# Performance work log

Measured on AMD Instinct MI355X. Metric: run time of the kernel, lower is better.

## Reference

```python
import jax, jax.numpy as jnp
import numpy as np

N_ATOMS = 50000
N_EDGES = 640000
D = 128
N_RBF = 20
N_INTER = 3

act = jax.nn.softplus


def setup_inputs() -> dict:
    key = jax.random.key(0)
    ks = jax.random.split(key, 16)
    s = 1.0 / np.sqrt(D)
    inp = {
        "x": jax.random.normal(ks[0], (N_ATOMS, D), jnp.float32),
        "g_ij": jax.random.uniform(ks[1], (N_EDGES, N_RBF), jnp.float32),
        "idx_i": jax.random.randint(ks[2], (N_EDGES,), 0, N_ATOMS),
        "idx_j": jax.random.randint(ks[3], (N_EDGES,), 0, N_ATOMS),
        "n_atoms": N_ATOMS,
        "u": jnp.ones((D,), jnp.float32),
        "Wf": jax.random.normal(ks[4], (D, D), jnp.float32) * s,
        "bf": jnp.zeros((D,), jnp.float32),
        # linear_g weight init to zero in original; use small random so grads flow
        "Wg": jax.random.normal(ks[5], (D, N_RBF), jnp.float32) * 0.01,
        "bg": jnp.zeros((D,), jnp.float32),
        "Wj": jax.random.normal(ks[6], (D, D), jnp.float32) * s,
        "bj": jnp.zeros((D,), jnp.float32),
        "Wi": jax.random.normal(ks[7], (D, D), jnp.float32) * s,
        "bi": jnp.zeros((D,), jnp.float32),
        "res_w1": jax.random.normal(ks[8], (N_INTER, D, D), jnp.float32) * s,
        "res_b1": jnp.zeros((N_INTER, D), jnp.float32),
        "res_w2": jax.random.normal(ks[9], (N_INTER, D, D), jnp.float32) * s,
        "res_b2": jnp.zeros((N_INTER, D), jnp.float32),
    }
    return inp


def reference(x, g_ij, idx_i, idx_j, n_atoms, u, Wf, bf, Wg, bg, Wj, bj, Wi, bi,
              res_w1, res_b1, res_w2, res_b2):
    x_j = x[idx_j]                                    # [E, D] gather
    xp = u * x                                        # [N, D]
    # sequential_j: act -> linear_j -> act, gated by linear_g(g_ij)
    vp = act(act(x_j) @ Wj.T + bj) * (g_ij @ Wg.T + bg)   # [E, D]
    vm = act(act(x) @ Wi.T + bi)                      # [N, D]
    v = jax.ops.segment_sum(vp, idx_i, num_segments=n_atoms) + vm
    for l in range(res_w1.shape[0]):
        h = act(v) @ res_w1[l].T + res_b1[l]
        h = act(h) @ res_w2[l].T + res_b2[l]
        v = h + v
    v = act(v)
    return xp + v @ Wf.T + bf
```

## Files before the change

### kernel.cpp

```cpp
#include <hip/hip_runtime.h>

#define DD 128

typedef __attribute__((ext_vector_type(8))) short short8;
typedef __attribute__((ext_vector_type(8))) unsigned short ushort8;
typedef __attribute__((ext_vector_type(4))) float floatx4;
typedef unsigned int uint32;

__device__ __forceinline__ float sp(float x) {
    return fmaxf(x, 0.0f) + __logf(1.0f + __expf(-fabsf(x)));
}

__device__ __forceinline__ unsigned short f2bf(float f) {
    union { float f; uint32 u; } c; c.f = f;
    const uint32 u = c.u;
    return (unsigned short)((u + 0x7fffu + ((u >> 16) & 1u)) >> 16);
}

__global__ __launch_bounds__(256)
void convert_w(const float* __restrict__ Wj, const float* __restrict__ Wi,
               const float* __restrict__ rw1, const float* __restrict__ rw2,
               const float* __restrict__ Wf, unsigned short* __restrict__ out)
{
    const int gid = blockIdx.x * 256 + threadIdx.x;
    if (gid >= 9 * 2048) return;
    const int mat = gid >> 11;
    const int f8  = gid & 2047;
    const float* src;
    if      (mat == 0) src = Wj;
    else if (mat == 1) src = Wi;
    else if (mat <= 4) src = rw1 + (size_t)(mat - 2) * 16384;
    else if (mat <= 7) src = rw2 + (size_t)(mat - 5) * 16384;
    else               src = Wf;
    const int row = f8 >> 4;
    const int ch  = f8 & 15;
    const float4 a = reinterpret_cast<const float4*>(src)[2 * f8];
    const float4 b = reinterpret_cast<const float4*>(src)[2 * f8 + 1];
    ushort8 u8;
    u8[0] = f2bf(a.x); u8[1] = f2bf(a.y); u8[2] = f2bf(a.z); u8[3] = f2bf(a.w);
    u8[4] = f2bf(b.x); u8[5] = f2bf(b.y); u8[6] = f2bf(b.z); u8[7] = f2bf(b.w);
    *reinterpret_cast<ushort8*>(out + (size_t)mat * 16384 + row * 128 +
                                ((ch ^ (row & 15)) << 3)) = u8;
}

__device__ __forceinline__ void stage_wb(const unsigned short* __restrict__ Wb,
                                         unsigned short* wl, int t)
{
    #pragma unroll
    for (int i = 0; i < 8; ++i) {
        const int c = t + i * 256;
        *reinterpret_cast<ushort8*>(wl + c * 8) =
            *reinterpret_cast<const ushort8*>(Wb + c * 8);
    }
}

__device__ __forceinline__ void load_afrag_act(const float* __restrict__ X,
                                               int m, int q, int n, short8 af[4])
{
    const int mm = m < n ? m : n - 1;
    const float* row = X + (size_t)mm * DD + q * 8;
    #pragma unroll
    for (int kk = 0; kk < 4; ++kk) {
        const float4 a = *reinterpret_cast<const float4*>(row + kk * 32);
        const float4 b = *reinterpret_cast<const float4*>(row + kk * 32 + 4);
        ushort8 u;
        u[0] = f2bf(sp(a.x)); u[1] = f2bf(sp(a.y)); u[2] = f2bf(sp(a.z)); u[3] = f2bf(sp(a.w));
        u[4] = f2bf(sp(b.x)); u[5] = f2bf(sp(b.y)); u[6] = f2bf(sp(b.z)); u[7] = f2bf(sp(b.w));
        af[kk] = __builtin_bit_cast(short8, u);
    }
}

__device__ __forceinline__ void mfma_gemm(const unsigned short* wl,
                                          const short8 af[4],
                                          int cl, int q, floatx4 acc[8])
{
    #pragma unroll
    for (int nt = 0; nt < 8; ++nt) {
        const int nrow = nt * 16 + cl;
        #pragma unroll
        for (int kk = 0; kk < 4; ++kk) {
            const int chs = (kk * 4 + q) ^ cl;
            const short8 bfr = *reinterpret_cast<const short8*>(wl + nrow * 128 + (chs << 3));
            acc[nt] = __builtin_amdgcn_mfma_f32_16x16x32_bf16(af[kk], bfr, acc[nt], 0, 0, 0);
        }
    }
}

__global__ __launch_bounds__(256, 4)
void dual_gemm(const float* __restrict__ x,
               const unsigned short* __restrict__ Wb,
               const float* __restrict__ bj, const float* __restrict__ bi,
               unsigned short* __restrict__ Aout, float* __restrict__ vout, int n)
{
    __shared__ __align__(16) unsigned short wl[128 * 128];
    const int t = threadIdx.x;
    const int lane = t & 63, wv = t >> 6;
    const int cl = lane & 15, q = lane >> 4;
    const int m0 = blockIdx.x * 64 + wv * 16;

    short8 af[4];
    load_afrag_act(x, m0 + cl, q, n, af);

    stage_wb(Wb, wl, t);
    __syncthreads();

    floatx4 acc[8];
    #pragma unroll
    for (int nt = 0; nt < 8; ++nt) acc[nt] = (floatx4){0.f, 0.f, 0.f, 0.f};
    mfma_gemm(wl, af, cl, q, acc);

    #pragma unroll
    for (int nt = 0; nt < 8; ++nt) {
        const int col = nt * 16 + cl;
        const float bb = bj[col];
        #pragma unroll
        for (int r = 0; r < 4; ++r) {
            const int row = m0 + q * 4 + r;
            if (row < n) Aout[(size_t)row * DD + col] = f2bf(sp(acc[nt][r] + bb));
        }
    }

    __syncthreads();
    stage_wb(Wb + 16384, wl, t);
    __syncthreads();

    #pragma unroll
    for (int nt = 0; nt < 8; ++nt) acc[nt] = (floatx4){0.f, 0.f, 0.f, 0.f};
    mfma_gemm(wl, af, cl, q, acc);

    #pragma unroll
    for (int nt = 0; nt < 8; ++nt) {
        const int col = nt * 16 + cl;
        const float bb = bi[col];
        #pragma unroll
        for (int r = 0; r < 4; ++r) {
            const int row = m0 + q * 4 + r;
            if (row < n) vout[(size_t)row * DD + col] = sp(acc[nt][r] + bb);
        }
    }
}

__global__ __launch_bounds__(256, 2)
void tail_kernel(const float* __restrict__ vin, const float* __restrict__ x,
                 const unsigned short* __restrict__ Wb,
                 const float* __restrict__ rb1, const float* __restrict__ rb2,
                 const float* __restrict__ bf, const float* __restrict__ u,
                 float* __restrict__ out, int n)
{
    __shared__ __align__(16) unsigned short wl[128 * 128];
    __shared__ __align__(16) unsigned short hl[64 * 128];
    __shared__ __align__(16) float vt[64 * 128];
    const int t = threadIdx.x;
    const int lane = t & 63, wv = t >> 6;
    const int cl = lane & 15, q = lane >> 4;
    const int mb = blockIdx.x * 64;

    #pragma unroll
    for (int i = 0; i < 8; ++i) {
        const int c = t + i * 256;
        const int row = c >> 5;
        const int chv = c & 31;
        float4 val = make_float4(0.f, 0.f, 0.f, 0.f);
        if (mb + row < n) val = reinterpret_cast<const float4*>(vin)[(size_t)mb * 32 + c];
        *reinterpret_cast<float4*>(vt + row * 128 + ((chv ^ (row & 15)) << 2)) = val;
    }
    stage_wb(Wb + 2 * 16384, wl, t);
    __syncthreads();

    floatx4 vac[8];
    #pragma unroll
    for (int nt = 0; nt < 8; ++nt) {
        #pragma unroll
        for (int r = 0; r < 4; ++r) {
            const int rl = wv * 16 + q * 4 + r;
            const int col = nt * 16 + cl;
            const int chv = col >> 2;
            vac[nt][r] = vt[rl * 128 + ((chv ^ (rl & 15)) << 2) + (col & 3)];
        }
    }

    short8 af[4];
    {
        const int rl = wv * 16 + cl;
        #pragma unroll
        for (int kk = 0; kk < 4; ++kk) {
            const int c0 = q * 2 + kk * 8;
            const floatx4 A0 = *reinterpret_cast<const floatx4*>(vt + rl * 128 + (((c0    ) ^ cl) << 2));
            const floatx4 A1 = *reinterpret_cast<const floatx4*>(vt + rl * 128 + (((c0 + 1) ^ cl) << 2));
            ushort8 u8;
            u8[0] = f2bf(sp(A0[0])); u8[1] = f2bf(sp(A0[1])); u8[2] = f2bf(sp(A0[2])); u8[3] = f2bf(sp(A0[3]));
            u8[4] = f2bf(sp(A1[0])); u8[5] = f2bf(sp(A1[1])); u8[6] = f2bf(sp(A1[2])); u8[7] = f2bf(sp(A1[3]));
            af[kk] = __builtin_bit_cast(short8, u8);
        }
    }

    const int ml2 = wv * 16 + cl;

    for (int l = 0; l < 3; ++l) {
        if (l > 0) {
            #pragma unroll
            for (int nt = 0; nt < 8; ++nt) {
                const int col = nt * 16 + cl;
                const int ch = col >> 3;
                #pragma unroll
                for (int r = 0; r < 4; ++r) {
                    const int ml = wv * 16 + q * 4 + r;
                    hl[ml * 128 + ((ch ^ (ml & 15)) << 3) + (col & 7)] = f2bf(sp(vac[nt][r]));
                }
            }
            #pragma unroll
            for (int kk = 0; kk < 4; ++kk)
                af[kk] = *reinterpret_cast<const short8*>(hl + ml2 * 128 + (((kk * 4 + q) ^ cl) << 3));
            __syncthreads();
            stage_wb(Wb + (size_t)(2 + l) * 16384, wl, t);
            __syncthreads();
        }

        floatx4 acc[8];
        #pragma unroll
        for (int nt = 0; nt < 8; ++nt) acc[nt] = (floatx4){0.f, 0.f, 0.f, 0.f};
        mfma_gemm(wl, af, cl, q, acc);

        const float* b1 = rb1 + (size_t)l * DD;
        #pragma unroll
        for (int nt = 0; nt < 8; ++nt) {
            const int col = nt * 16 + cl;
            const int ch = col >> 3;
            const float bb = b1[col];
            #pragma unroll
            for (int r = 0; r < 4; ++r) {
                const int ml = wv * 16 + q * 4 + r;
                hl[ml * 128 + ((ch ^ (ml & 15)) << 3) + (col & 7)] = f2bf(sp(acc[nt][r] + bb));
            }
        }
        short8 af2[4];
        #pragma unroll
        for (int kk = 0; kk < 4; ++kk)
            af2[kk] = *reinterpret_cast<const short8*>(hl + ml2 * 128 + (((kk * 4 + q) ^ cl) << 3));

        __syncthreads();
        stage_wb(Wb + (size_t)(5 + l) * 16384, wl, t);
        __syncthreads();

        #pragma unroll
        for (int nt = 0; nt < 8; ++nt) acc[nt] = (floatx4){0.f, 0.f, 0.f, 0.f};
        mfma_gemm(wl, af2, cl, q, acc);

        const float* b2 = rb2 + (size_t)l * DD;
        #pragma unroll
        for (int nt = 0; nt < 8; ++nt) {
            const float bb = b2[nt * 16 + cl];
            #pragma unroll
            for (int r = 0; r < 4; ++r) vac[nt][r] += acc[nt][r] + bb;
        }
    }

    __syncthreads();
    stage_wb(Wb + (size_t)8 * 16384, wl, t);
    #pragma unroll
    for (int i = 0; i < 8; ++i) {
        const int c = t + i * 256;
        const int row = c >> 5;
        const int chv = c & 31;
        float4 val = make_float4(0.f, 0.f, 0.f, 0.f);
        if (mb + row < n) val = reinterpret_cast<const float4*>(x)[(size_t)mb * 32 + c];
        *reinterpret_cast<float4*>(vt + row * 128 + ((chv ^ (row & 15)) << 2)) = val;
    }
    __syncthreads();

    #pragma unroll
    for (int nt = 0; nt < 8; ++nt) {
        const int col = nt * 16 + cl;
        const int ch = col >> 3;
        #pragma unroll
        for (int r = 0; r < 4; ++r) {
            const int ml = wv * 16 + q * 4 + r;
            hl[ml * 128 + ((ch ^ (ml & 15)) << 3) + (col & 7)] = f2bf(sp(vac[nt][r]));
        }
    }
    short8 aff[4];
    #pragma unroll
    for (int kk = 0; kk < 4; ++kk)
        aff[kk] = *reinterpret_cast<const short8*>(hl + ml2 * 128 + (((kk * 4 + q) ^ cl) << 3));

    floatx4 acc[8];
    #pragma unroll
    for (int nt = 0; nt < 8; ++nt) acc[nt] = (floatx4){0.f, 0.f, 0.f, 0.f};
    mfma_gemm(wl, aff, cl, q, acc);

    #pragma unroll
    for (int nt = 0; nt < 8; ++nt) {
        const int col = nt * 16 + cl;
        const float bb = bf[col];
        const float uu = u[col];
        const int chv = col >> 2;
        #pragma unroll
        for (int r = 0; r < 4; ++r) {
            const int rl = wv * 16 + q * 4 + r;
            const int row = mb + rl;
            if (row < n) {
                const float xv = vt[rl * 128 + ((chv ^ (rl & 15)) << 2) + (col & 3)];
                out[(size_t)row * DD + col] = acc[nt][r] + bb + uu * xv;
            }
        }
    }
}


__global__ __launch_bounds__(256)
void hist_kernel(const int* __restrict__ idx_i, int* __restrict__ cnt, int E)
{
    const int e = blockIdx.x * 256 + threadIdx.x;
    if (e < E) atomicAdd(&cnt[idx_i[e]], 1);
}

__global__ __launch_bounds__(256)
void scan_reduce(const int* __restrict__ cnt, int* __restrict__ bsum, int n)
{
    __shared__ int wsum[4];
    const int t = threadIdx.x;
    const int lane = t & 63, wv = t >> 6;
    const int i0 = blockIdx.x * 1024 + t * 4;
    int s = 0;
    #pragma unroll
    for (int k = 0; k < 4; ++k) if (i0 + k < n) s += cnt[i0 + k];
    #pragma unroll
    for (int d = 1; d < 64; d <<= 1) s += __shfl_down(s, d, 64);
    if (lane == 0) wsum[wv] = s;
    __syncthreads();
    if (t == 0) bsum[blockIdx.x] = wsum[0] + wsum[1] + wsum[2] + wsum[3];
}

__global__ __launch_bounds__(64)
void scan_partials(int* __restrict__ bsum, int nb)
{
    const int t = threadIdx.x;
    int v = (t < nb) ? bsum[t] : 0;
    int incl = v;
    #pragma unroll
    for (int d = 1; d < 64; d <<= 1) {
        const int y = __shfl_up(incl, d, 64);
        if (t >= d) incl += y;
    }
    if (t < nb) bsum[t] = incl - v;
}

__global__ __launch_bounds__(256)
void scan_apply(const int* __restrict__ cnt, const int* __restrict__ bsum,
                int* __restrict__ off, int* __restrict__ cnt2, int n)
{
    __shared__ int wsum[4];
    const int t = threadIdx.x;
    const int lane = t & 63, wv = t >> 6;
    const int i0 = blockIdx.x * 1024 + t * 4;
    const int v0 = (i0 + 0 < n) ? cnt[i0 + 0] : 0;
    const int v1 = (i0 + 1 < n) ? cnt[i0 + 1] : 0;
    const int v2 = (i0 + 2 < n) ? cnt[i0 + 2] : 0;
    const int v3 = (i0 + 3 < n) ? cnt[i0 + 3] : 0;
    const int s = v0 + v1 + v2 + v3;
    int incl = s;
    #pragma unroll
    for (int d = 1; d < 64; d <<= 1) {
        const int y = __shfl_up(incl, d, 64);
        if (lane >= d) incl += y;
    }
    if (lane == 63) wsum[wv] = incl;
    __syncthreads();
    int woff = bsum[blockIdx.x];
    #pragma unroll
    for (int w = 0; w < 4; ++w) if (w < wv) woff += wsum[w];
    const int excl = woff + incl - s;
    if (i0 + 0 < n) { off[i0 + 0] = excl;                cnt2[i0 + 0] = 0; }
    if (i0 + 1 < n) { off[i0 + 1] = excl + v0;           cnt2[i0 + 1] = 0; }
    if (i0 + 2 < n) { off[i0 + 2] = excl + v0 + v1;      cnt2[i0 + 2] = 0; }
    if (i0 + 3 < n) { off[i0 + 3] = excl + v0 + v1 + v2; cnt2[i0 + 3] = 0; }
}

__global__ __launch_bounds__(256)
void scatter_kernel(const int* __restrict__ idx_i, const int* __restrict__ idx_j,
                    const int* __restrict__ off, int* __restrict__ cnt2,
                    int2* __restrict__ spair, int E)
{
    const int e = blockIdx.x * 256 + threadIdx.x;
    if (e < E) {
        const int i = idx_i[e];
        const int p = off[i] + atomicAdd(&cnt2[i], 1);
        spair[p] = make_int2(e, idx_j[e]);
    }
}

__global__ __launch_bounds__(256, 4)
void agg_kernel(const int* __restrict__ off, const int* __restrict__ cnt,
                const int2* __restrict__ spair,
                const float* __restrict__ g,
                const float* __restrict__ Wg, const float* __restrict__ bg,
                const unsigned short* __restrict__ A, float* __restrict__ v, int N)
{
    const int t = threadIdx.x;
    const int lane = t & 63;
    const int wid0 = blockIdx.x * 4 + (t >> 6);
    const int nw   = gridDim.x * 4;
    const int d0 = lane << 1;

    float2 wg01[20];
    #pragma unroll
    for (int k = 0; k < 20; ++k) {
        wg01[k].x = Wg[d0 * 20 + k];
        wg01[k].y = Wg[(d0 + 1) * 20 + k];
    }
    const float bg0 = bg[d0], bg1 = bg[d0 + 1];

    for (int i = wid0; i < N; i += nw) {
        const int beg = off[i], num = cnt[i], end = beg + num;

        float2 acc = *reinterpret_cast<const float2*>(v + (size_t)i * DD + d0);

        int p = beg;
        for (; p + 2 <= end; p += 2) {
            const int2 pr0 = spair[p];
            const int2 pr1 = spair[p + 1];
            const int e0 = __builtin_amdgcn_readfirstlane(pr0.x);
            const int j0 = __builtin_amdgcn_readfirstlane(pr0.y);
            const int e1 = __builtin_amdgcn_readfirstlane(pr1.x);
            const int j1 = __builtin_amdgcn_readfirstlane(pr1.y);
            const uint32 a0 = *reinterpret_cast<const uint32*>(A + (size_t)j0 * DD + d0);
            const uint32 a1 = *reinterpret_cast<const uint32*>(A + (size_t)j1 * DD + d0);
            const float4* g0p = reinterpret_cast<const float4*>(g + (size_t)e0 * 20);
            const float4* g1p = reinterpret_cast<const float4*>(g + (size_t)e1 * 20);
            float2 t0 = make_float2(bg0, bg1), t1 = make_float2(bg0, bg1);
            #pragma unroll
            for (int qq = 0; qq < 5; ++qq) {
                const float4 p0 = g0p[qq];
                const float4 p1 = g1p[qq];
                t0.x = fmaf(p0.x, wg01[qq*4+0].x, t0.x); t0.y = fmaf(p0.x, wg01[qq*4+0].y, t0.y);
                t0.x = fmaf(p0.y, wg01[qq*4+1].x, t0.x); t0.y = fmaf(p0.y, wg01[qq*4+1].y, t0.y);
                t0.x = fmaf(p0.z, wg01[qq*4+2].x, t0.x); t0.y = fmaf(p0.z, wg01[qq*4+2].y, t0.y);
                t0.x = fmaf(p0.w, wg01[qq*4+3].x, t0.x); t0.y = fmaf(p0.w, wg01[qq*4+3].y, t0.y);
                t1.x = fmaf(p1.x, wg01[qq*4+0].x, t1.x); t1.y = fmaf(p1.x, wg01[qq*4+0].y, t1.y);
                t1.x = fmaf(p1.y, wg01[qq*4+1].x, t1.x); t1.y = fmaf(p1.y, wg01[qq*4+1].y, t1.y);
                t1.x = fmaf(p1.z, wg01[qq*4+2].x, t1.x); t1.y = fmaf(p1.z, wg01[qq*4+2].y, t1.y);
                t1.x = fmaf(p1.w, wg01[qq*4+3].x, t1.x); t1.y = fmaf(p1.w, wg01[qq*4+3].y, t1.y);
            }
            union { uint32 u; float f; } c0x, c0y, c1x, c1y;
            c0x.u = a0 << 16; c0y.u = a0 & 0xffff0000u;
            c1x.u = a1 << 16; c1y.u = a1 & 0xffff0000u;
            acc.x = fmaf(c0x.f, t0.x, acc.x); acc.y = fmaf(c0y.f, t0.y, acc.y);
            acc.x = fmaf(c1x.f, t1.x, acc.x); acc.y = fmaf(c1y.f, t1.y, acc.y);
        }
        if (p < end) {
            const int2 pr0 = spair[p];
            const int e0 = __builtin_amdgcn_readfirstlane(pr0.x);
            const int j0 = __builtin_amdgcn_readfirstlane(pr0.y);
            const uint32 a0 = *reinterpret_cast<const uint32*>(A + (size_t)j0 * DD + d0);
            const float4* g0p = reinterpret_cast<const float4*>(g + (size_t)e0 * 20);
            float2 t0 = make_float2(bg0, bg1);
            #pragma unroll
            for (int qq = 0; qq < 5; ++qq) {
                const float4 p0 = g0p[qq];
                t0.x = fmaf(p0.x, wg01[qq*4+0].x, t0.x); t0.y = fmaf(p0.x, wg01[qq*4+0].y, t0.y);
                t0.x = fmaf(p0.y, wg01[qq*4+1].x, t0.x); t0.y = fmaf(p0.y, wg01[qq*4+1].y, t0.y);
                t0.x = fmaf(p0.z, wg01[qq*4+2].x, t0.x); t0.y = fmaf(p0.z, wg01[qq*4+2].y, t0.y);
                t0.x = fmaf(p0.w, wg01[qq*4+3].x, t0.x); t0.y = fmaf(p0.w, wg01[qq*4+3].y, t0.y);
            }
            union { uint32 u; float f; } c0x, c0y;
            c0x.u = a0 << 16; c0y.u = a0 & 0xffff0000u;
            acc.x = fmaf(c0x.f, t0.x, acc.x); acc.y = fmaf(c0y.f, t0.y, acc.y);
        }
        *reinterpret_cast<float2*>(v + (size_t)i * DD + d0) = acc;
    }
}

extern "C" void kernel_launch(void* const* d_in, const int* in_sizes, int n_in,
                              void* d_out, int out_size, void* d_ws, size_t ws_size,
                              hipStream_t stream)
{
    const float* x     = (const float*)d_in[0];
    const float* g     = (const float*)d_in[1];
    const int*   idx_i = (const int*)d_in[2];
    const int*   idx_j = (const int*)d_in[3];
    const float* u     = (const float*)d_in[5];
    const float* Wf    = (const float*)d_in[6];
    const float* bf    = (const float*)d_in[7];
    const float* Wg    = (const float*)d_in[8];
    const float* bg    = (const float*)d_in[9];
    const float* Wj    = (const float*)d_in[10];
    const float* bj    = (const float*)d_in[11];
    const float* Wi    = (const float*)d_in[12];
    const float* bi    = (const float*)d_in[13];
    const float* rw1   = (const float*)d_in[14];
    const float* rb1   = (const float*)d_in[15];
    const float* rw2   = (const float*)d_in[16];
    const float* rb2   = (const float*)d_in[17];

    const int N = in_sizes[0] / DD;
    const int E = in_sizes[2];
    float* out = (float*)d_out;

    float*          v     = (float*)d_ws;
    unsigned short* A     = (unsigned short*)(v + (size_t)N * DD);
    int*            cnt   = (int*)(A + (size_t)N * DD);
    int*            off   = cnt + N;
    int*            cnt2  = off + N;
    int*            bsum  = cnt2 + N;
    int2*           spair = (int2*)(bsum + 64);
    unsigned short* Wb    = (unsigned short*)(spair + E);

    dim3 blk(256);
    const int tiles    = (N + 63) / 64;
    const int eblocks  = (E + 255) / 256;
    const int sblocks  = (N + 1023) / 1024;

    convert_w<<<72, blk, 0, stream>>>(Wj, Wi, rw1, rw2, Wf, Wb);

    hipMemsetAsync(cnt, 0, (size_t)N * sizeof(int), stream);
    hist_kernel<<<eblocks, blk, 0, stream>>>(idx_i, cnt, E);
    scan_reduce<<<sblocks, blk, 0, stream>>>(cnt, bsum, N);
    scan_partials<<<1, 64, 0, stream>>>(bsum, sblocks);
    scan_apply<<<sblocks, blk, 0, stream>>>(cnt, bsum, off, cnt2, N);
    scatter_kernel<<<eblocks, blk, 0, stream>>>(idx_i, idx_j, off, cnt2, spair, E);

    dual_gemm<<<tiles, blk, 0, stream>>>(x, Wb, bj, bi, A, v, N);

    agg_kernel<<<2048, blk, 0, stream>>>(off, cnt, spair, g, Wg, bg, A, v, N);

    tail_kernel<<<tiles, blk, 0, stream>>>(v, x, Wb, rb1, rb2, bf, u, out, N);
}
```

Measured before the change: 255.5 us.

## Store g_ij as fp16 and compute the edge gate with packed half FMAs

New measurement: 242.7 us. 1.05x faster.

```diff
diff --git a/kernel.cpp b/kernel.cpp
--- a/kernel.cpp
+++ b/kernel.cpp
@@ -1,4 +1,5 @@
 #include <hip/hip_runtime.h>
+#include <hip/hip_fp16.h>
 
 #define DD 128
 
@@ -17,13 +18,31 @@
     return (unsigned short)((u + 0x7fffu + ((u >> 16) & 1u)) >> 16);
 }
 
+__device__ __forceinline__ unsigned short f2h(float f) {
+    __half h = __float2half(f);
+    return __builtin_bit_cast(unsigned short, h);
+}
+
 __global__ __launch_bounds__(256)
 void convert_w(const float* __restrict__ Wj, const float* __restrict__ Wi,
                const float* __restrict__ rw1, const float* __restrict__ rw2,
-               const float* __restrict__ Wf, unsigned short* __restrict__ out)
-{
+               const float* __restrict__ Wf, unsigned short* __restrict__ out,
+               const float* __restrict__ g, unsigned short* __restrict__ gh,
+               int gchunks)
+{
+    if ((int)blockIdx.x >= 72) {
+        const int gid = ((int)blockIdx.x - 72) * 256 + threadIdx.x;
+        if (gid < gchunks) {
+            const float4 f0 = reinterpret_cast<const float4*>(g)[2 * gid];
+            const float4 f1 = reinterpret_cast<const float4*>(g)[2 * gid + 1];
+            ushort8 o;
+            o[0] = f2h(f0.x); o[1] = f2h(f0.y); o[2] = f2h(f0.z); o[3] = f2h(f0.w);
+            o[4] = f2h(f1.x); o[5] = f2h(f1.y); o[6] = f2h(f1.z); o[7] = f2h(f1.w);
+            reinterpret_cast<ushort8*>(gh)[gid] = o;
+        }
+        return;
+    }
     const int gid = blockIdx.x * 256 + threadIdx.x;
-    if (gid >= 9 * 2048) return;
     const int mat = gid >> 11;
     const int f8  = gid & 2047;
     const float* src;
@@ -331,27 +350,19 @@
     if (t == 0) bsum[blockIdx.x] = wsum[0] + wsum[1] + wsum[2] + wsum[3];
 }
 
-__global__ __launch_bounds__(64)
-void scan_partials(int* __restrict__ bsum, int nb)
-{
-    const int t = threadIdx.x;
-    int v = (t < nb) ? bsum[t] : 0;
-    int incl = v;
-    #pragma unroll
-    for (int d = 1; d < 64; d <<= 1) {
-        const int y = __shfl_up(incl, d, 64);
-        if (t >= d) incl += y;
-    }
-    if (t < nb) bsum[t] = incl - v;
-}
-
 __global__ __launch_bounds__(256)
 void scan_apply(const int* __restrict__ cnt, const int* __restrict__ bsum,
-                int* __restrict__ off, int* __restrict__ cnt2, int n)
+                int* __restrict__ off, int* __restrict__ cnt2, int n, int nb)
 {
     __shared__ int wsum[4];
     const int t = threadIdx.x;
     const int lane = t & 63, wv = t >> 6;
+
+    int bval = (lane < nb && lane < (int)blockIdx.x) ? bsum[lane] : 0;
+    #pragma unroll
+    for (int d = 32; d >= 1; d >>= 1) bval += __shfl_down(bval, d, 64);
+    const int blk_off = __shfl(bval, 0, 64);
+
     const int i0 = blockIdx.x * 1024 + t * 4;
     const int v0 = (i0 + 0 < n) ? cnt[i0 + 0] : 0;
     const int v1 = (i0 + 1 < n) ? cnt[i0 + 1] : 0;
@@ -366,7 +377,7 @@
     }
     if (lane == 63) wsum[wv] = incl;
     __syncthreads();
-    int woff = bsum[blockIdx.x];
+    int woff = blk_off;
     #pragma unroll
     for (int w = 0; w < 4; ++w) if (w < wv) woff += wsum[w];
     const int excl = woff + incl - s;
@@ -389,9 +400,11 @@
     }
 }
 
+template<int GH>
 __global__ __launch_bounds__(256, 4)
 void agg_kernel(const int* __restrict__ off, const int* __restrict__ cnt,
                 const int2* __restrict__ spair,
+                const unsigned short* __restrict__ gh,
                 const float* __restrict__ g,
                 const float* __restrict__ Wg, const float* __restrict__ bg,
                 const unsigned short* __restrict__ A, float* __restrict__ v, int N)
@@ -402,71 +415,150 @@
     const int nw   = gridDim.x * 4;
     const int d0 = lane << 1;
 
-    float2 wg01[20];
-    #pragma unroll
-    for (int k = 0; k < 20; ++k) {
-        wg01[k].x = Wg[d0 * 20 + k];
-        wg01[k].y = Wg[(d0 + 1) * 20 + k];
-    }
     const float bg0 = bg[d0], bg1 = bg[d0 + 1];
 
-    for (int i = wid0; i < N; i += nw) {
-        const int beg = off[i], num = cnt[i], end = beg + num;
-
-        float2 acc = *reinterpret_cast<const float2*>(v + (size_t)i * DD + d0);
-
-        int p = beg;
-        for (; p + 2 <= end; p += 2) {
-            const int2 pr0 = spair[p];
-            const int2 pr1 = spair[p + 1];
-            const int e0 = __builtin_amdgcn_readfirstlane(pr0.x);
-            const int j0 = __builtin_amdgcn_readfirstlane(pr0.y);
-            const int e1 = __builtin_amdgcn_readfirstlane(pr1.x);
-            const int j1 = __builtin_amdgcn_readfirstlane(pr1.y);
-            const uint32 a0 = *reinterpret_cast<const uint32*>(A + (size_t)j0 * DD + d0);
-            const uint32 a1 = *reinterpret_cast<const uint32*>(A + (size_t)j1 * DD + d0);
-            const float4* g0p = reinterpret_cast<const float4*>(g + (size_t)e0 * 20);
-            const float4* g1p = reinterpret_cast<const float4*>(g + (size_t)e1 * 20);
-            float2 t0 = make_float2(bg0, bg1), t1 = make_float2(bg0, bg1);
-            #pragma unroll
-            for (int qq = 0; qq < 5; ++qq) {
-                const float4 p0 = g0p[qq];
-                const float4 p1 = g1p[qq];
-                t0.x = fmaf(p0.x, wg01[qq*4+0].x, t0.x); t0.y = fmaf(p0.x, wg01[qq*4+0].y, t0.y);
-                t0.x = fmaf(p0.y, wg01[qq*4+1].x, t0.x); t0.y = fmaf(p0.y, wg01[qq*4+1].y, t0.y);
-                t0.x = fmaf(p0.z, wg01[qq*4+2].x, t0.x); t0.y = fmaf(p0.z, wg01[qq*4+2].y, t0.y);
-                t0.x = fmaf(p0.w, wg01[qq*4+3].x, t0.x); t0.y = fmaf(p0.w, wg01[qq*4+3].y, t0.y);
-                t1.x = fmaf(p1.x, wg01[qq*4+0].x, t1.x); t1.y = fmaf(p1.x, wg01[qq*4+0].y, t1.y);
-                t1.x = fmaf(p1.y, wg01[qq*4+1].x, t1.x); t1.y = fmaf(p1.y, wg01[qq*4+1].y, t1.y);
-                t1.x = fmaf(p1.z, wg01[qq*4+2].x, t1.x); t1.y = fmaf(p1.z, wg01[qq*4+2].y, t1.y);
-                t1.x = fmaf(p1.w, wg01[qq*4+3].x, t1.x); t1.y = fmaf(p1.w, wg01[qq*4+3].y, t1.y);
+    if (GH) {
+        __half2 w0h[10], w1h[10];
+        #pragma unroll
+        for (int k2 = 0; k2 < 10; ++k2) {
+            w0h[k2] = __floats2half2_rn(Wg[d0 * 20 + 2 * k2], Wg[d0 * 20 + 2 * k2 + 1]);
+            w1h[k2] = __floats2half2_rn(Wg[(d0 + 1) * 20 + 2 * k2], Wg[(d0 + 1) * 20 + 2 * k2 + 1]);
+        }
+
+        for (int i = wid0; i < N; i += nw) {
+            const int beg = off[i], num = cnt[i], end = beg + num;
+            float2 acc = *reinterpret_cast<const float2*>(v + (size_t)i * DD + d0);
+
+            int p = beg;
+            while (p + 4 <= end) {
+                int ee[4], jj[4];
+                #pragma unroll
+                for (int u = 0; u < 4; ++u) {
+                    const int2 pr = spair[p + u];
+                    ee[u] = __builtin_amdgcn_readfirstlane(pr.x);
+                    jj[u] = __builtin_amdgcn_readfirstlane(pr.y);
+                }
+                uint32 aa[4];
+                float2 gq[4][5];
+                #pragma unroll
+                for (int u = 0; u < 4; ++u) {
+                    aa[u] = *reinterpret_cast<const uint32*>(A + (size_t)jj[u] * DD + d0);
+                    const float2* gp = reinterpret_cast<const float2*>(gh + (size_t)ee[u] * 20);
+                    #pragma unroll
+                    for (int q2 = 0; q2 < 5; ++q2) gq[u][q2] = gp[q2];
+                }
+                #pragma unroll
+                for (int u = 0; u < 4; ++u) {
+                    __half2 a0 = __float2half2_rn(0.f), a1 = __float2half2_rn(0.f);
+                    #pragma unroll
+                    for (int q2 = 0; q2 < 5; ++q2) {
+                        const __half2 h0 = __builtin_bit_cast(__half2, gq[u][q2].x);
+                        const __half2 h1 = __builtin_bit_cast(__half2, gq[u][q2].y);
+                        a0 = __hfma2(h0, w0h[2 * q2], a0);
+                        a1 = __hfma2(h0, w1h[2 * q2], a1);
+                        a0 = __hfma2(h1, w0h[2 * q2 + 1], a0);
+                        a1 = __hfma2(h1, w1h[2 * q2 + 1], a1);
+                    }
+                    const float t0 = bg0 + __low2float(a0) + __high2float(a0);
+                    const float t1 = bg1 + __low2float(a1) + __high2float(a1);
+                    union { uint32 u32; float f; } cx, cy;
+                    cx.u32 = aa[u] << 16;
+                    cy.u32 = aa[u] & 0xffff0000u;
+                    acc.x = fmaf(cx.f, t0, acc.x);
+                    acc.y = fmaf(cy.f, t1, acc.y);
+                }
+                p += 4;
             }
-            union { uint32 u; float f; } c0x, c0y, c1x, c1y;
-            c0x.u = a0 << 16; c0y.u = a0 & 0xffff0000u;
-            c1x.u = a1 << 16; c1y.u = a1 & 0xffff0000u;
-            acc.x = fmaf(c0x.f, t0.x, acc.x); acc.y = fmaf(c0y.f, t0.y, acc.y);
-            acc.x = fmaf(c1x.f, t1.x, acc.x); acc.y = fmaf(c1y.f, t1.y, acc.y);
-        }
-        if (p < end) {
-            const int2 pr0 = spair[p];
-            const int e0 = __builtin_amdgcn_readfirstlane(pr0.x);
-            const int j0 = __builtin_amdgcn_readfirstlane(pr0.y);
-            const uint32 a0 = *reinterpret_cast<const uint32*>(A + (size_t)j0 * DD + d0);
-            const float4* g0p = reinterpret_cast<const float4*>(g + (size_t)e0 * 20);
-            float2 t0 = make_float2(bg0, bg1);
-            #pragma unroll
-            for (int qq = 0; qq < 5; ++qq) {
-                const float4 p0 = g0p[qq];
-                t0.x = fmaf(p0.x, wg01[qq*4+0].x, t0.x); t0.y = fmaf(p0.x, wg01[qq*4+0].y, t0.y);
-                t0.x = fmaf(p0.y, wg01[qq*4+1].x, t0.x); t0.y = fmaf(p0.y, wg01[qq*4+1].y, t0.y);
-                t0.x = fmaf(p0.z, wg01[qq*4+2].x, t0.x); t0.y = fmaf(p0.z, wg01[qq*4+2].y, t0.y);
-                t0.x = fmaf(p0.w, wg01[qq*4+3].x, t0.x); t0.y = fmaf(p0.w, wg01[qq*4+3].y, t0.y);
+            for (; p < end; ++p) {
+                const int2 pr = spair[p];
+                const int e0 = __builtin_amdgcn_readfirstlane(pr.x);
+                const int j0 = __builtin_amdgcn_readfirstlane(pr.y);
+                const uint32 a0u = *reinterpret_cast<const uint32*>(A + (size_t)j0 * DD + d0);
+                const float2* gp = reinterpret_cast<const float2*>(gh + (size_t)e0 * 20);
+                __half2 a0 = __float2half2_rn(0.f), a1 = __float2half2_rn(0.f);
+                #pragma unroll
+                for (int q2 = 0; q2 < 5; ++q2) {
+                    const float2 qq = gp[q2];
+                    const __half2 h0 = __builtin_bit_cast(__half2, qq.x);
+                    const __half2 h1 = __builtin_bit_cast(__half2, qq.y);
+                    a0 = __hfma2(h0, w0h[2 * q2], a0);
+                    a1 = __hfma2(h0, w1h[2 * q2], a1);
+                    a0 = __hfma2(h1, w0h[2 * q2 + 1], a0);
+                    a1 = __hfma2(h1, w1h[2 * q2 + 1], a1);
+                }
+                const float t0 = bg0 + __low2float(a0) + __high2float(a0);
+                const float t1 = bg1 + __low2float(a1) + __high2float(a1);
+                union { uint32 u32; float f; } cx, cy;
+                cx.u32 = a0u << 16;
+                cy.u32 = a0u & 0xffff0000u;
+                acc.x = fmaf(cx.f, t0, acc.x);
+                acc.y = fmaf(cy.f, t1, acc.y);
             }
-            union { uint32 u; float f; } c0x, c0y;
-            c0x.u = a0 << 16; c0y.u = a0 & 0xffff0000u;
-            acc.x = fmaf(c0x.f, t0.x, acc.x); acc.y = fmaf(c0y.f, t0.y, acc.y);
-        }
-        *reinterpret_cast<float2*>(v + (size_t)i * DD + d0) = acc;
+            *reinterpret_cast<float2*>(v + (size_t)i * DD + d0) = acc;
+        }
+    } else {
+        float2 wg01[20];
+        #pragma unroll
+        for (int k = 0; k < 20; ++k) {
+            wg01[k].x = Wg[d0 * 20 + k];
+            wg01[k].y = Wg[(d0 + 1) * 20 + k];
+        }
+        for (int i = wid0; i < N; i += nw) {
+            const int beg = off[i], num = cnt[i], end = beg + num;
+            float2 acc = *reinterpret_cast<const float2*>(v + (size_t)i * DD + d0);
+            int p = beg;
+            for (; p + 2 <= end; p += 2) {
+                const int2 pr0 = spair[p];
+                const int2 pr1 = spair[p + 1];
+                const int e0 = __builtin_amdgcn_readfirstlane(pr0.x);
+                const int j0 = __builtin_amdgcn_readfirstlane(pr0.y);
+                const int e1 = __builtin_amdgcn_readfirstlane(pr1.x);
+                const int j1 = __builtin_amdgcn_readfirstlane(pr1.y);
+                const uint32 a0 = *reinterpret_cast<const uint32*>(A + (size_t)j0 * DD + d0);
+                const uint32 a1 = *reinterpret_cast<const uint32*>(A + (size_t)j1 * DD + d0);
+                const float4* g0p = reinterpret_cast<const float4*>(g + (size_t)e0 * 20);
+                const float4* g1p = reinterpret_cast<const float4*>(g + (size_t)e1 * 20);
+                float2 t0 = make_float2(bg0, bg1), t1 = make_float2(bg0, bg1);
+                #pragma unroll
+                for (int qq = 0; qq < 5; ++qq) {
+                    const float4 p0 = g0p[qq];
+                    const float4 p1 = g1p[qq];
+                    t0.x = fmaf(p0.x, wg01[qq*4+0].x, t0.x); t0.y = fmaf(p0.x, wg01[qq*4+0].y, t0.y);
+                    t0.x = fmaf(p0.y, wg01[qq*4+1].x, t0.x); t0.y = fmaf(p0.y, wg01[qq*4+1].y, t0.y);
+                    t0.x = fmaf(p0.z, wg01[qq*4+2].x, t0.x); t0.y = fmaf(p0.z, wg01[qq*4+2].y, t0.y);
+                    t0.x = fmaf(p0.w, wg01[qq*4+3].x, t0.x); t0.y = fmaf(p0.w, wg01[qq*4+3].y, t0.y);
+                    t1.x = fmaf(p1.x, wg01[qq*4+0].x, t1.x); t1.y = fmaf(p1.x, wg01[qq*4+0].y, t1.y);
+                    t1.x = fmaf(p1.y, wg01[qq*4+1].x, t1.x); t1.y = fmaf(p1.y, wg01[qq*4+1].y, t1.y);
+                    t1.x = fmaf(p1.z, wg01[qq*4+2].x, t1.x); t1.y = fmaf(p1.z, wg01[qq*4+2].y, t1.y);
+                    t1.x = fmaf(p1.w, wg01[qq*4+3].x, t1.x); t1.y = fmaf(p1.w, wg01[qq*4+3].y, t1.y);
+                }
+                union { uint32 u; float f; } c0x, c0y, c1x, c1y;
+                c0x.u = a0 << 16; c0y.u = a0 & 0xffff0000u;
+                c1x.u = a1 << 16; c1y.u = a1 & 0xffff0000u;
+                acc.x = fmaf(c0x.f, t0.x, acc.x); acc.y = fmaf(c0y.f, t0.y, acc.y);
+                acc.x = fmaf(c1x.f, t1.x, acc.x); acc.y = fmaf(c1y.f, t1.y, acc.y);
+            }
+            if (p < end) {
+                const int2 pr0 = spair[p];
+                const int e0 = __builtin_amdgcn_readfirstlane(pr0.x);
+                const int j0 = __builtin_amdgcn_readfirstlane(pr0.y);
+                const uint32 a0 = *reinterpret_cast<const uint32*>(A + (size_t)j0 * DD + d0);
+                const float4* g0p = reinterpret_cast<const float4*>(g + (size_t)e0 * 20);
+                float2 t0 = make_float2(bg0, bg1);
+                #pragma unroll
+                for (int qq = 0; qq < 5; ++qq) {
+                    const float4 p0 = g0p[qq];
+                    t0.x = fmaf(p0.x, wg01[qq*4+0].x, t0.x); t0.y = fmaf(p0.x, wg01[qq*4+0].y, t0.y);
+                    t0.x = fmaf(p0.y, wg01[qq*4+1].x, t0.x); t0.y = fmaf(p0.y, wg01[qq*4+1].y, t0.y);
+                    t0.x = fmaf(p0.z, wg01[qq*4+2].x, t0.x); t0.y = fmaf(p0.z, wg01[qq*4+2].y, t0.y);
+                    t0.x = fmaf(p0.w, wg01[qq*4+3].x, t0.x); t0.y = fmaf(p0.w, wg01[qq*4+3].y, t0.y);
+                }
+                union { uint32 u; float f; } c0x, c0y;
+                c0x.u = a0 << 16; c0y.u = a0 & 0xffff0000u;
+                acc.x = fmaf(c0x.f, t0.x, acc.x); acc.y = fmaf(c0y.f, t0.y, acc.y);
+            }
+            *reinterpret_cast<float2*>(v + (size_t)i * DD + d0) = acc;
+        }
     }
 }
 
@@ -504,24 +596,35 @@
     int*            bsum  = cnt2 + N;
     int2*           spair = (int2*)(bsum + 64);
     unsigned short* Wb    = (unsigned short*)(spair + E);
+    unsigned short* gh    = Wb + 9 * 16384;
+
+    const size_t need_gh = (size_t)((char*)(gh + (size_t)E * 20) - (char*)d_ws);
+    const bool gh_ok = ws_size >= need_gh;
 
     dim3 blk(256);
     const int tiles    = (N + 63) / 64;
     const int eblocks  = (E + 255) / 256;
     const int sblocks  = (N + 1023) / 1024;
-
-    convert_w<<<72, blk, 0, stream>>>(Wj, Wi, rw1, rw2, Wf, Wb);
+    const int gchunks  = gh_ok ? (E * 20) / 8 : 0;
+    const int gblocks  = gh_ok ? (gchunks + 255) / 256 : 0;
+
+    convert_w<<<72 + gblocks, blk, 0, stream>>>(Wj, Wi, rw1, rw2, Wf, Wb,
+                                                g, gh, gchunks);
 
     hipMemsetAsync(cnt, 0, (size_t)N * sizeof(int), stream);
     hist_kernel<<<eblocks, blk, 0, stream>>>(idx_i, cnt, E);
     scan_reduce<<<sblocks, blk, 0, stream>>>(cnt, bsum, N);
-    scan_partials<<<1, 64, 0, stream>>>(bsum, sblocks);
-    scan_apply<<<sblocks, blk, 0, stream>>>(cnt, bsum, off, cnt2, N);
+    scan_apply<<<sblocks, blk, 0, stream>>>(cnt, bsum, off, cnt2, N, sblocks);
     scatter_kernel<<<eblocks, blk, 0, stream>>>(idx_i, idx_j, off, cnt2, spair, E);
 
     dual_gemm<<<tiles, blk, 0, stream>>>(x, Wb, bj, bi, A, v, N);
 
-    agg_kernel<<<2048, blk, 0, stream>>>(off, cnt, spair, g, Wg, bg, A, v, N);
+    if (gh_ok)
+        agg_kernel<1><<<2048, blk, 0, stream>>>(off, cnt, spair, gh, g,
+                                                Wg, bg, A, v, N);
+    else
+        agg_kernel<0><<<2048, blk, 0, stream>>>(off, cnt, spair, gh, g,
+                                                Wg, bg, A, v, N);
 
     tail_kernel<<<tiles, blk, 0, stream>>>(v, x, Wb, rb1, rb2, bf, u, out, N);
 }
```
